# Optimization experiments

Measured on AMD Instinct MI355X. Metric: run time of the kernel, lower is better.

## Reference

```python
import jax, jax.numpy as jnp
import numpy as np

# near_sym_a (5,7)-tap biorthogonal analysis filters used by DTCWT level 1
_H0O = np.array([-0.05, 0.25, 0.5, 0.25, -0.05], dtype=np.float32)
_H1O = np.array([-0.0107143, 0.0535714, 0.2607143, -0.6071429,
                 0.2607143, 0.0535714, -0.0107143], dtype=np.float32)

MAGBIAS = np.float32(0.01)


def _filt(x, h, axis):
    """Depthwise 1D correlation of NCHW x along `axis` (2=H rows, 3=W cols)
    with symmetric (half-sample reflect) padding; output same spatial size
    (odd-length filters)."""
    m = h.shape[0] // 2
    pad = [(0, 0)] * 4
    pad[axis] = (m, m)
    xp = jnp.pad(x, pad, mode='symmetric')
    n, c, hh, ww = xp.shape
    k = h.reshape(1, 1, -1, 1) if axis == 2 else h.reshape(1, 1, 1, -1)
    y = jax.lax.conv_general_dilated(
        xp.reshape(n * c, 1, hh, ww), k, (1, 1), 'VALID',
        dimension_numbers=('NCHW', 'OIHW', 'NCHW'))
    return y.reshape(n, c, y.shape[2], y.shape[3])


def _q2c(y):
    # quads -> two complex subimages: ((a-d) + j(b+c), (a+d) + j(b-c)) / sqrt(2)
    y = y * np.float32(1.0 / np.sqrt(2.0))
    a = y[..., 0::2, 0::2]
    b = y[..., 0::2, 1::2]
    c = y[..., 1::2, 0::2]
    d = y[..., 1::2, 1::2]
    return (a - d, b + c), (a + d, b - c)


def _scat_j1(x, h0o, h1o, magbias):
    # level-1 DTCWT: separable biorthogonal filtering (no decimation)
    lo = _filt(x, h0o, 3)   # row lowpass  (along W)
    hi = _filt(x, h1o, 3)   # row highpass
    ll = _filt(lo, h0o, 2)  # (N,C,H,W) lowpass
    lh = _filt(lo, h1o, 2)
    hl = _filt(hi, h0o, 2)
    hh = _filt(hi, h1o, 2)
    # quads -> 6 oriented complex subbands at half resolution
    (d15r, d15i), (d165r, d165i) = _q2c(lh)
    (d45r, d45i), (d135r, d135i) = _q2c(hh)
    (d75r, d75i), (d105r, d105i) = _q2c(hl)
    reals = jnp.stack([d15r, d45r, d75r, d105r, d135r, d165r], axis=1)  # (N,6,C,H/2,W/2)
    imags = jnp.stack([d15i, d45i, d75i, d105i, d135i, d165i], axis=1)
    # smoothed complex magnitude nonlinearity
    r = jnp.sqrt(reals * reals + imags * imags + magbias * magbias) - magbias
    # 2x2 average pool of lowpass
    n, c, hh_, ww_ = ll.shape
    ll = ll.reshape(n, c, hh_ // 2, 2, ww_ // 2, 2).mean(axis=(3, 5))
    b_, _, c_, h_, w_ = r.shape
    r = r.reshape(b_, 6 * c_, h_, w_)
    return ll, r


def setup_inputs() -> dict:
    key = jax.random.key(0)
    x = jax.random.normal(key, (32, 64, 128, 128), dtype=jnp.float32)
    # non-trainable wavelet filter "parameters" (fixed near_sym_a taps)
    return {"x": x, "h0o": jnp.asarray(_H0O), "h1o": jnp.asarray(_H1O)}


def reference(x, h0o, h1o):
    # H, W are even here so the odd-size edge-replication branch is a no-op
    return _scat_j1(x, h0o, h1o, MAGBIAS)
```

## Files before the change

kernel.cpp:

```cpp
#include <hip/hip_runtime.h>
#include <math.h>

#define HALO 3
#define TILE_IN 32
#define LROWS (TILE_IN + 2*HALO)
#define W 128
#define TILE_OUT 16

__device__ __forceinline__ int refl128(int i) {
    i = (i < 0) ? (-1 - i) : i;
    return (i > 127) ? (255 - i) : i;
}

__device__ __forceinline__ float2 vdot7(const float2* A) {
    float2 r;
    r.x = fmaf(-0.0107143f, A[0].x + A[6].x,
          fmaf( 0.0535714f, A[1].x + A[5].x,
          fmaf( 0.2607143f, A[2].x + A[4].x, -0.6071429f * A[3].x)));
    r.y = fmaf(-0.0107143f, A[0].y + A[6].y,
          fmaf( 0.0535714f, A[1].y + A[5].y,
          fmaf( 0.2607143f, A[2].y + A[4].y, -0.6071429f * A[3].y)));
    return r;
}

__device__ __forceinline__ float2 vdot5(const float2* A) {
    float2 r;
    r.x = fmaf(-0.05f, A[0].x + A[4].x, fmaf(0.25f, A[1].x + A[3].x, 0.5f * A[2].x));
    r.y = fmaf(-0.05f, A[0].y + A[4].y, fmaf(0.25f, A[1].y + A[3].y, 0.5f * A[2].y));
    return r;
}

__device__ __forceinline__ float magf(float re, float im) {
    return sqrtf(fmaf(re, re, fmaf(im, im, 1.0e-4f))) - 0.01f;
}

__global__ __launch_bounds__(256) void scat_j1_kernel(
    const float* __restrict__ x,
    float* __restrict__ out_ll,
    float* __restrict__ out_r)
{
    __shared__ float slo[LROWS][W];
    __shared__ float shi[LROWS][W];

    const int bid   = blockIdx.x;
    const int plane = bid >> 2;
    const int tile  = bid & 3;
    const int r0    = tile * TILE_IN;
    const int tid   = threadIdx.x;

    const float* __restrict__ xp = x + (size_t)plane * (W * W);

    {
        const int g  = tid & 31;
        const int rb = tid >> 5;
        #pragma unroll
        for (int it = 0; it < 5; ++it) {
            const int lr = it * 8 + rb;
            if (lr < LROWS) {
                const int q = refl128(r0 - HALO + lr);
                const float4* __restrict__ rv = (const float4*)(xp + (size_t)q * W);
                const float4 B = rv[g];
                float4 A = rv[g > 0 ? g - 1 : 0];
                float4 C = rv[g < 31 ? g + 1 : 31];
                const float4 revB = make_float4(B.w, B.z, B.y, B.x);
                if (g == 0)  A = revB;
                if (g == 31) C = revB;
                const float wv[10] = {A.y, A.z, A.w, B.x, B.y, B.z, B.w, C.x, C.y, C.z};
                float4 lo4, hi4;
                float* lop = &lo4.x;
                float* hip_ = &hi4.x;
                #pragma unroll
                for (int j = 0; j < 4; ++j) {
                    const float sA = wv[j]     + wv[j + 6];
                    const float sB = wv[j + 1] + wv[j + 5];
                    const float sC = wv[j + 2] + wv[j + 4];
                    const float ct = wv[j + 3];
                    lop[j]  = fmaf(-0.05f, sB, fmaf(0.25f, sC, 0.5f * ct));
                    hip_[j] = fmaf(-0.0107143f, sA,
                              fmaf( 0.0535714f, sB,
                              fmaf( 0.2607143f, sC, -0.6071429f * ct)));
                }
                ((float4*)&slo[lr][0])[g] = lo4;
                ((float4*)&shi[lr][0])[g] = hi4;
            }
        }
    }
    __syncthreads();

    const int J     = tid & 63;
    const int Ib    = tid >> 6;
    const int c0    = 2 * J;
    const int n     = plane >> 6;
    const int ch    = plane & 63;
    const int Rbase = Ib * 8;
    const float S   = 0.70710678118654752f;

    float2 L[8], H[8];
    #pragma unroll
    for (int t = 0; t < 8; ++t) {
        L[t] = *(const float2*)&slo[Rbase + t][c0];
        H[t] = *(const float2*)&shi[Rbase + t][c0];
    }

    #pragma unroll
    for (int k = 0; k < 4; ++k) {
        const float2 lh_t = vdot7(L);
        const float2 lh_b = vdot7(L + 1);
        const float2 ll_t = vdot5(L + 1);
        const float2 ll_b = vdot5(L + 2);
        const float2 hh_t = vdot7(H);
        const float2 hh_b = vdot7(H + 1);
        const float2 hl_t = vdot5(H + 1);
        const float2 hl_b = vdot5(H + 2);

        float a, b, c_, d;
        a = S * lh_t.x; b = S * lh_t.y; c_ = S * lh_b.x; d = S * lh_b.y;
        const float m15  = magf(a - d, b + c_);
        const float m165 = magf(a + d, b - c_);
        a = S * hh_t.x; b = S * hh_t.y; c_ = S * hh_b.x; d = S * hh_b.y;
        const float m45  = magf(a - d, b + c_);
        const float m135 = magf(a + d, b - c_);
        a = S * hl_t.x; b = S * hl_t.y; c_ = S * hl_b.x; d = S * hl_b.y;
        const float m75  = magf(a - d, b + c_);
        const float m105 = magf(a + d, b - c_);

        const int Il = Ib * 4 + k;
        const int I  = tile * TILE_OUT + Il;

        __builtin_nontemporal_store(
            0.25f * (ll_t.x + ll_t.y + ll_b.x + ll_b.y),
            &out_ll[(size_t)plane * 4096 + I * 64 + J]);

        float* rb_p = out_r + ((size_t)(n * 384 + ch)) * 4096 + (size_t)I * 64 + J;
        __builtin_nontemporal_store(m15,  rb_p + 0u * 262144);
        __builtin_nontemporal_store(m45,  rb_p + 1u * 262144);
        __builtin_nontemporal_store(m75,  rb_p + 2u * 262144);
        __builtin_nontemporal_store(m105, rb_p + 3u * 262144);
        __builtin_nontemporal_store(m135, rb_p + 4u * 262144);
        __builtin_nontemporal_store(m165, rb_p + 5u * 262144);

        if (k < 3) {
            #pragma unroll
            for (int t = 0; t < 6; ++t) { L[t] = L[t + 2]; H[t] = H[t + 2]; }
            const int rn = Rbase + 8 + 2 * k;
            L[6] = *(const float2*)&slo[rn][c0];
            L[7] = *(const float2*)&slo[rn + 1][c0];
            H[6] = *(const float2*)&shi[rn][c0];
            H[7] = *(const float2*)&shi[rn + 1][c0];
        }
    }
}

extern "C" void kernel_launch(void* const* d_in, const int* in_sizes, int n_in,
                              void* d_out, int out_size, void* d_ws, size_t ws_size,
                              hipStream_t stream) {
    const float* x = (const float*)d_in[0];
    float* out = (float*)d_out;
    float* out_ll = out;
    float* out_r  = out + 8388608;

    dim3 grid(2048 * 4);
    dim3 block(256);
    hipLaunchKernelGGL(scat_j1_kernel, grid, block, 0, stream, x, out_ll, out_r);
}
```

Measured before the change: 78.69 us.

## Replace shared-memory staging with register sliding window over row strips

Each block now handles a whole 128x128 plane, and each warp-sized group of 32 threads walks a 16-row strip. Every thread row-filters its own float4 columns straight from global memory into a register sliding window, so the shared-memory tile and the barrier are gone. The 2x2 output quad pairs are written as float2 nontemporal stores, and the sqrt(2) scale is folded into the filter coefficients. The costs are fewer blocks (2048 instead of 8192), more registers per thread from holding float4 windows, and redundant halo rows loaded per strip straight from global or cache.

```diff
diff --git a/kernel.cpp b/kernel.cpp
--- a/kernel.cpp
+++ b/kernel.cpp
@@ -1,37 +1,104 @@
 #include <hip/hip_runtime.h>
 #include <math.h>
 
-#define HALO 3
-#define TILE_IN 32
-#define LROWS (TILE_IN + 2*HALO)
 #define W 128
-#define TILE_OUT 16
+
+typedef float f2_t __attribute__((ext_vector_type(2)));
 
 __device__ __forceinline__ int refl128(int i) {
     i = (i < 0) ? (-1 - i) : i;
     return (i > 127) ? (255 - i) : i;
 }
 
-__device__ __forceinline__ float2 vdot7(const float2* A) {
-    float2 r;
-    r.x = fmaf(-0.0107143f, A[0].x + A[6].x,
-          fmaf( 0.0535714f, A[1].x + A[5].x,
-          fmaf( 0.2607143f, A[2].x + A[4].x, -0.6071429f * A[3].x)));
-    r.y = fmaf(-0.0107143f, A[0].y + A[6].y,
-          fmaf( 0.0535714f, A[1].y + A[5].y,
-          fmaf( 0.2607143f, A[2].y + A[4].y, -0.6071429f * A[3].y)));
+__device__ __forceinline__ float magf(float re, float im) {
+    return sqrtf(fmaf(re, re, fmaf(im, im, 1.0e-4f))) - 0.01f;
+}
+
+__device__ __forceinline__ void st2(float* p, float a, float b) {
+    f2_t v;
+    v.x = a; v.y = b;
+    __builtin_nontemporal_store(v, (f2_t*)p);
+}
+
+__device__ __forceinline__ float4 d7(float4 A, float4 B, float4 C, float4 D,
+                                     float4 E, float4 F, float4 G,
+                                     float k0, float k1, float k2, float k3) {
+    float4 r;
+    r.x = fmaf(k0, A.x + G.x, fmaf(k1, B.x + F.x, fmaf(k2, C.x + E.x, k3 * D.x)));
+    r.y = fmaf(k0, A.y + G.y, fmaf(k1, B.y + F.y, fmaf(k2, C.y + E.y, k3 * D.y)));
+    r.z = fmaf(k0, A.z + G.z, fmaf(k1, B.z + F.z, fmaf(k2, C.z + E.z, k3 * D.z)));
+    r.w = fmaf(k0, A.w + G.w, fmaf(k1, B.w + F.w, fmaf(k2, C.w + E.w, k3 * D.w)));
     return r;
 }
 
-__device__ __forceinline__ float2 vdot5(const float2* A) {
-    float2 r;
-    r.x = fmaf(-0.05f, A[0].x + A[4].x, fmaf(0.25f, A[1].x + A[3].x, 0.5f * A[2].x));
-    r.y = fmaf(-0.05f, A[0].y + A[4].y, fmaf(0.25f, A[1].y + A[3].y, 0.5f * A[2].y));
+__device__ __forceinline__ float4 d5(float4 A, float4 B, float4 C, float4 D, float4 E,
+                                     float k0, float k1, float k2) {
+    float4 r;
+    r.x = fmaf(k0, A.x + E.x, fmaf(k1, B.x + D.x, k2 * C.x));
+    r.y = fmaf(k0, A.y + E.y, fmaf(k1, B.y + D.y, k2 * C.y));
+    r.z = fmaf(k0, A.z + E.z, fmaf(k1, B.z + D.z, k2 * C.z));
+    r.w = fmaf(k0, A.w + E.w, fmaf(k1, B.w + D.w, k2 * C.w));
     return r;
 }
 
-__device__ __forceinline__ float magf(float re, float im) {
-    return sqrtf(fmaf(re, re, fmaf(im, im, 1.0e-4f))) - 0.01f;
+struct Row { float4 lo, hi; };
+
+__device__ __forceinline__ Row hfilt(const float4* __restrict__ rv, int g) {
+    const float4 B = rv[g];
+    float4 A = rv[g > 0 ? g - 1 : 0];
+    float4 C = rv[g < 31 ? g + 1 : 31];
+    const float4 revB = make_float4(B.w, B.z, B.y, B.x);
+    if (g == 0)  A = revB;
+    if (g == 31) C = revB;
+    const float wv[10] = {A.y, A.z, A.w, B.x, B.y, B.z, B.w, C.x, C.y, C.z};
+    Row r;
+    float* lop  = &r.lo.x;
+    float* hip_ = &r.hi.x;
+    #pragma unroll
+    for (int j = 0; j < 4; ++j) {
+        const float sA = wv[j]     + wv[j + 6];
+        const float sB = wv[j + 1] + wv[j + 5];
+        const float sC = wv[j + 2] + wv[j + 4];
+        const float ct = wv[j + 3];
+        lop[j]  = fmaf(-0.05f, sB, fmaf(0.25f, sC, 0.5f * ct));
+        hip_[j] = fmaf(-0.0107143f, sA,
+                  fmaf( 0.0535714f, sB,
+                  fmaf( 0.2607143f, sC, -0.6071429f * ct)));
+    }
+    return r;
+}
+
+__device__ __forceinline__ void emit(const float4 (&L)[8], const float4 (&H)[8],
+                                     float* __restrict__ llp,
+                                     float* __restrict__ rp) {
+    const float S  = 0.70710678118654752f;
+    const float a7 = -0.0107143f * S, b7 = 0.0535714f * S,
+                c7 =  0.2607143f * S, d7c = -0.6071429f * S;
+    const float a5 = -0.05f * S, b5 = 0.25f * S, c5 = 0.5f * S;
+
+    {
+        const float4 t  = d7(L[0], L[1], L[2], L[3], L[4], L[5], L[6], a7, b7, c7, d7c);
+        const float4 bo = d7(L[1], L[2], L[3], L[4], L[5], L[6], L[7], a7, b7, c7, d7c);
+        st2(rp + 0u * 262144u, magf(t.x - bo.y, t.y + bo.x), magf(t.z - bo.w, t.w + bo.z));
+        st2(rp + 5u * 262144u, magf(t.x + bo.y, t.y - bo.x), magf(t.z + bo.w, t.w - bo.z));
+    }
+    {
+        const float4 t  = d5(L[1], L[2], L[3], L[4], L[5], -0.0125f, 0.0625f, 0.125f);
+        const float4 bo = d5(L[2], L[3], L[4], L[5], L[6], -0.0125f, 0.0625f, 0.125f);
+        st2(llp, (t.x + t.y) + (bo.x + bo.y), (t.z + t.w) + (bo.z + bo.w));
+    }
+    {
+        const float4 t  = d7(H[0], H[1], H[2], H[3], H[4], H[5], H[6], a7, b7, c7, d7c);
+        const float4 bo = d7(H[1], H[2], H[3], H[4], H[5], H[6], H[7], a7, b7, c7, d7c);
+        st2(rp + 1u * 262144u, magf(t.x - bo.y, t.y + bo.x), magf(t.z - bo.w, t.w + bo.z));
+        st2(rp + 4u * 262144u, magf(t.x + bo.y, t.y - bo.x), magf(t.z + bo.w, t.w - bo.z));
+    }
+    {
+        const float4 t  = d5(H[1], H[2], H[3], H[4], H[5], a5, b5, c5);
+        const float4 bo = d5(H[2], H[3], H[4], H[5], H[6], a5, b5, c5);
+        st2(rp + 2u * 262144u, magf(t.x - bo.y, t.y + bo.x), magf(t.z - bo.w, t.w + bo.z));
+        st2(rp + 3u * 262144u, magf(t.x + bo.y, t.y - bo.x), magf(t.z + bo.w, t.w - bo.z));
+    }
 }
 
 __global__ __launch_bounds__(256) void scat_j1_kernel(
@@ -39,115 +106,48 @@
     float* __restrict__ out_ll,
     float* __restrict__ out_r)
 {
-    __shared__ float slo[LROWS][W];
-    __shared__ float shi[LROWS][W];
-
-    const int bid   = blockIdx.x;
-    const int plane = bid >> 2;
-    const int tile  = bid & 3;
-    const int r0    = tile * TILE_IN;
     const int tid   = threadIdx.x;
+    const int g     = tid & 31;
+    const int strip = tid >> 5;
+    const int plane = blockIdx.x;
+    const int n     = plane >> 6;
+    const int ch    = plane & 63;
+    const int r0    = strip * 16;
 
     const float* __restrict__ xp = x + (size_t)plane * (W * W);
 
-    {
-        const int g  = tid & 31;
-        const int rb = tid >> 5;
+    float4 L[8], H[8];
+
+    #pragma unroll
+    for (int p = 0; p < 4; ++p) {
         #pragma unroll
-        for (int it = 0; it < 5; ++it) {
-            const int lr = it * 8 + rb;
-            if (lr < LROWS) {
-                const int q = refl128(r0 - HALO + lr);
-                const float4* __restrict__ rv = (const float4*)(xp + (size_t)q * W);
-                const float4 B = rv[g];
-                float4 A = rv[g > 0 ? g - 1 : 0];
-                float4 C = rv[g < 31 ? g + 1 : 31];
-                const float4 revB = make_float4(B.w, B.z, B.y, B.x);
-                if (g == 0)  A = revB;
-                if (g == 31) C = revB;
-                const float wv[10] = {A.y, A.z, A.w, B.x, B.y, B.z, B.w, C.x, C.y, C.z};
-                float4 lo4, hi4;
-                float* lop = &lo4.x;
-                float* hip_ = &hi4.x;
-                #pragma unroll
-                for (int j = 0; j < 4; ++j) {
-                    const float sA = wv[j]     + wv[j + 6];
-                    const float sB = wv[j + 1] + wv[j + 5];
-                    const float sC = wv[j + 2] + wv[j + 4];
-                    const float ct = wv[j + 3];
-                    lop[j]  = fmaf(-0.05f, sB, fmaf(0.25f, sC, 0.5f * ct));
-                    hip_[j] = fmaf(-0.0107143f, sA,
-                              fmaf( 0.0535714f, sB,
-                              fmaf( 0.2607143f, sC, -0.6071429f * ct)));
-                }
-                ((float4*)&slo[lr][0])[g] = lo4;
-                ((float4*)&shi[lr][0])[g] = hi4;
-            }
+        for (int s = 0; s < 2; ++s) {
+            const int q = refl128(r0 - 3 + 2 * p + s);
+            const Row rr = hfilt((const float4*)(xp + (size_t)q * W), g);
+            L[2 * p + s] = rr.lo;
+            H[2 * p + s] = rr.hi;
         }
     }
-    __syncthreads();
 
-    const int J     = tid & 63;
-    const int Ib    = tid >> 6;
-    const int c0    = 2 * J;
-    const int n     = plane >> 6;
-    const int ch    = plane & 63;
-    const int Rbase = Ib * 8;
-    const float S   = 0.70710678118654752f;
+    float* llp = out_ll + (size_t)plane * 4096 + (size_t)(strip * 8) * 64 + 2 * g;
+    float* rp  = out_r + ((size_t)(n * 384 + ch)) * 4096 + (size_t)(strip * 8) * 64 + 2 * g;
 
-    float2 L[8], H[8];
-    #pragma unroll
-    for (int t = 0; t < 8; ++t) {
-        L[t] = *(const float2*)&slo[Rbase + t][c0];
-        H[t] = *(const float2*)&shi[Rbase + t][c0];
-    }
+    emit(L, H, llp, rp);
 
     #pragma unroll
-    for (int k = 0; k < 4; ++k) {
-        const float2 lh_t = vdot7(L);
-        const float2 lh_b = vdot7(L + 1);
-        const float2 ll_t = vdot5(L + 1);
-        const float2 ll_b = vdot5(L + 2);
-        const float2 hh_t = vdot7(H);
-        const float2 hh_b = vdot7(H + 1);
-        const float2 hl_t = vdot5(H + 1);
-        const float2 hl_b = vdot5(H + 2);
-
-        float a, b, c_, d;
-        a = S * lh_t.x; b = S * lh_t.y; c_ = S * lh_b.x; d = S * lh_b.y;
-        const float m15  = magf(a - d, b + c_);
-        const float m165 = magf(a + d, b - c_);
-        a = S * hh_t.x; b = S * hh_t.y; c_ = S * hh_b.x; d = S * hh_b.y;
-        const float m45  = magf(a - d, b + c_);
-        const float m135 = magf(a + d, b - c_);
-        a = S * hl_t.x; b = S * hl_t.y; c_ = S * hl_b.x; d = S * hl_b.y;
-        const float m75  = magf(a - d, b + c_);
-        const float m105 = magf(a + d, b - c_);
-
-        const int Il = Ib * 4 + k;
-        const int I  = tile * TILE_OUT + Il;
-
-        __builtin_nontemporal_store(
-            0.25f * (ll_t.x + ll_t.y + ll_b.x + ll_b.y),
-            &out_ll[(size_t)plane * 4096 + I * 64 + J]);
-
-        float* rb_p = out_r + ((size_t)(n * 384 + ch)) * 4096 + (size_t)I * 64 + J;
-        __builtin_nontemporal_store(m15,  rb_p + 0u * 262144);
-        __builtin_nontemporal_store(m45,  rb_p + 1u * 262144);
-        __builtin_nontemporal_store(m75,  rb_p + 2u * 262144);
-        __builtin_nontemporal_store(m105, rb_p + 3u * 262144);
-        __builtin_nontemporal_store(m135, rb_p + 4u * 262144);
-        __builtin_nontemporal_store(m165, rb_p + 5u * 262144);
-
-        if (k < 3) {
-            #pragma unroll
-            for (int t = 0; t < 6; ++t) { L[t] = L[t + 2]; H[t] = H[t + 2]; }
-            const int rn = Rbase + 8 + 2 * k;
-            L[6] = *(const float2*)&slo[rn][c0];
-            L[7] = *(const float2*)&slo[rn + 1][c0];
-            H[6] = *(const float2*)&shi[rn][c0];
-            H[7] = *(const float2*)&shi[rn + 1][c0];
+    for (int p = 4; p <= 10; ++p) {
+        #pragma unroll
+        for (int t = 0; t < 6; ++t) { L[t] = L[t + 2]; H[t] = H[t + 2]; }
+        #pragma unroll
+        for (int s = 0; s < 2; ++s) {
+            const int q = refl128(r0 - 3 + 2 * p + s);
+            const Row rr = hfilt((const float4*)(xp + (size_t)q * W), g);
+            L[6 + s] = rr.lo;
+            H[6 + s] = rr.hi;
         }
+        llp += 64;
+        rp  += 64;
+        emit(L, H, llp, rp);
     }
 }
 
@@ -159,7 +159,7 @@
     float* out_ll = out;
     float* out_r  = out + 8388608;
 
-    dim3 grid(2048 * 4);
+    dim3 grid(2048);
     dim3 block(256);
     hipLaunchKernelGGL(scat_j1_kernel, grid, block, 0, stream, x, out_ll, out_r);
 }
```

After: 96.41 us. 1.23x slower.
